# Performance work log

Measured on AMD Instinct MI355X. Metric: run time of the kernel, lower is better.

## Reference

```python
import jax, jax.numpy as jnp
import numpy as np

CLIP_LEN = 16
IN_CH = 64  # math.ceil(256 // 4 / 4) * 4
BN_EPS = 1e-5


def setup_inputs() -> dict:
    key = jax.random.key(0)
    ks = jax.random.split(key, 7)
    x = jax.random.normal(ks[0], (128, 256, 56, 56), jnp.float32)
    bn_gamma = 1.0 + 0.1 * jax.random.normal(ks[1], (IN_CH,), jnp.float32)
    bn_beta = 0.1 * jax.random.normal(ks[2], (IN_CH,), jnp.float32)
    bn_mean = 0.1 * jax.random.normal(ks[3], (IN_CH,), jnp.float32)
    bn_var = jax.random.uniform(ks[4], (IN_CH,), jnp.float32, minval=0.5, maxval=1.5)
    # groups=2 Conv3d: out=2, in_per_group=IN_CH//2, kernel 3x3x3
    conv_w = 0.02 * jax.random.normal(ks[5], (2, IN_CH // 2, 3, 3, 3), jnp.float32)
    conv_b = 0.02 * jax.random.normal(ks[6], (2,), jnp.float32)
    return dict(x=x, bn_gamma=bn_gamma, bn_beta=bn_beta, bn_mean=bn_mean,
                bn_var=bn_var, conv_w=conv_w, conv_b=conv_b)


def _gsm(x5, bn_gamma, bn_beta, bn_mean, bn_var, conv_w, conv_b):
    # x5: [n, c, t, h, w] with c == IN_CH
    n, c, t, h, w = x5.shape
    scale = bn_gamma * jax.lax.rsqrt(bn_var + BN_EPS)          # [c]
    shift = bn_beta - bn_mean * scale                          # [c]
    x_act = jax.nn.relu(x5 * scale[None, :, None, None, None]
                        + shift[None, :, None, None, None])
    gate = jnp.tanh(
        jax.lax.conv_general_dilated(
            x_act, conv_w, window_strides=(1, 1, 1), padding='SAME',
            dimension_numbers=('NCDHW', 'OIDHW', 'NCDHW'),
            feature_group_count=2)
        + conv_b[None, :, None, None, None])                   # [n,2,t,h,w]
    half = c // 2

    def gated_shift(xg, g, left):
        y = g * xg                                             # gated part
        r = xg - y                                             # residual part
        if left:
            y_sh = jnp.concatenate([y[:, :, 1:], jnp.zeros_like(y[:, :, :1])], axis=2)
        else:
            y_sh = jnp.concatenate([jnp.zeros_like(y[:, :, :1]), y[:, :, :-1]], axis=2)
        out = y_sh + r
        # channel regroup: [n,2,c/4,t,h,w] -> permute -> [n,c/2,t,h,w]
        return out.reshape(n, 2, half // 2, t, h, w).transpose(0, 2, 1, 3, 4, 5).reshape(n, half, t, h, w)

    y1 = gated_shift(x5[:, :half], gate[:, 0:1], left=True)
    y2 = gated_shift(x5[:, half:], gate[:, 1:2], left=False)
    return jnp.concatenate([y1, y2], axis=1)


def reference(x, bn_gamma, bn_beta, bn_mean, bn_var, conv_w, conv_b):
    nt, c, h, w = x.shape
    n = nt // CLIP_LEN
    # [nt, IN_CH, h, w] -> [n, IN_CH, T, h, w]
    xs = x[:, :IN_CH].reshape(n, CLIP_LEN, IN_CH, h, w).transpose(0, 2, 1, 3, 4)
    y = _gsm(xs, bn_gamma, bn_beta, bn_mean, bn_var, conv_w, conv_b)
    y = y.transpose(0, 2, 1, 3, 4).reshape(nt, IN_CH, h, w)
    # remaining channels pass through unchanged; net wrapper is identity
    return jnp.concatenate([y, x[:, IN_CH:]], axis=1)
```

## Files before the change

### kernel.cpp

```cpp
#include <hip/hip_runtime.h>
#include <math.h>

namespace {
constexpr int kT = 16;
constexpr int kH = 56;
constexpr int kW = 56;
constexpr int kCAll = 256;
constexpr int kPlane = kH * kW;
constexpr int kPlane4 = kPlane / 4;
constexpr size_t kGateBytes = (size_t)256 * kPlane * sizeof(float);
constexpr int kSpan = 192 * kPlane4;
constexpr int kFrame4 = kCAll * kPlane4;
}


__global__ __launch_bounds__(256, 2)
void fused_conv_copy_kernel(const float* __restrict__ x,
                            const float* __restrict__ gamma,
                            const float* __restrict__ beta,
                            const float* __restrict__ mean,
                            const float* __restrict__ var,
                            const float* __restrict__ cw,
                            const float* __restrict__ cb,
                            float* __restrict__ gate,
                            const float4* __restrict__ x4,
                            float4* __restrict__ o4,
                            int nf_copy, int skip_hole) {
  __shared__ float4 smb[4 * 510];

  if ((blockIdx.x & 1) == 0) {
    const int engine = blockIdx.x >> 1;
    const size_t stride = (size_t)512 * 256;
    const size_t total = (size_t)nf_copy * kSpan;
    size_t j = (size_t)engine * 256 + threadIdx.x;
    auto mapidx = [&](size_t jj, size_t& idx, bool& ok) {
      const int f = (int)(jj / kSpan);
      const int within = (int)(jj - (size_t)f * kSpan);
      ok = !(skip_hole && f == 126 && within < 3 * kPlane4);
      idx = (size_t)f * kFrame4 + 64 * kPlane4 + within;
    };
    for (; j + 3 * stride < total; j += 4 * stride) {
      size_t i0, i1, i2, i3; bool k0, k1, k2, k3;
      mapidx(j, i0, k0); mapidx(j + stride, i1, k1);
      mapidx(j + 2 * stride, i2, k2); mapidx(j + 3 * stride, i3, k3);
      const float4 a = x4[i0], b = x4[i1], c = x4[i2], d = x4[i3];
      if (k0) o4[i0] = a;
      if (k1) o4[i1] = b;
      if (k2) o4[i2] = c;
      if (k3) o4[i3] = d;
    }
    for (; j < total; j += stride) {
      size_t i0; bool k0;
      mapidx(j, i0, k0);
      const float4 a = x4[i0];
      if (k0) o4[i0] = a;
    }
    return;
  }

  const int bid = blockIdx.x >> 1;
  const int stripe = bid & 1;
  const int g = (bid >> 1) & 1;
  const int t = (bid >> 2) & 15;
  const int n = bid >> 6;
  const int h0 = stripe * 28;
  const int tid = threadIdx.x;
  const int wid = tid >> 6;
  const int lane = tid & 63;
  const int r = lane >> 1;
  const int h = lane & 1;
  const int wbase = wid * 510;

  for (int i = lane; i < 510; i += 64)
    smb[wbase + i] = make_float4(0.f, 0.f, 0.f, 0.f);

  int rr_u[7], fb_u[7], go_u[7];
  bool val_u[7];
  #pragma unroll
  for (int u = 0; u < 7; ++u) {
    const int j = lane + u * 64;
    bool v = (j < 420);
    int rr = 0, fb = 0, go = 0;
    if (v) {
      rr = j / 14;
      fb = j - rr * 14;
      const int gr = h0 + rr - 1;
      v = ((unsigned)gr < (unsigned)kH);
      if (v) go = gr * 14 + fb;
    }
    rr_u[u] = rr; fb_u[u] = fb; go_u[u] = go; val_u[u] = v;
  }

  float acc[28];
  #pragma unroll
  for (int p = 0; p < 28; ++p) acc[p] = 0.f;

  auto loadS = [&](int s, float4 (&pf)[7]) {
    const int il = s / 3;
    const int kd = s - il * 3;
    const int tt = t + kd - 1;
    const int ch = g * 32 + wid * 8 + il;
    if (tt >= 0 && tt < kT) {
      const float4* src4 =
          (const float4*)x + ((size_t)(n * kT + tt) * kCAll + ch) * kPlane4;
      #pragma unroll
      for (int u = 0; u < 7; ++u)
        pf[u] = val_u[u] ? src4[go_u[u]] : make_float4(0.f, 0.f, 0.f, 0.f);
    } else {
      #pragma unroll
      for (int u = 0; u < 7; ++u) pf[u] = make_float4(0.f, 0.f, 0.f, 0.f);
    }
  };

  auto stageS = [&](int s, const float4 (&pf)[7]) {
    const int il = s / 3;
    const int kd = s - il * 3;
    const int tt = t + kd - 1;
    if (tt < 0 || tt >= kT) return;
    const int ch = g * 32 + wid * 8 + il;
    const float sc = gamma[ch] * rsqrtf(var[ch] + 1e-5f);
    const float sh = beta[ch] - mean[ch] * sc;
    #pragma unroll
    for (int u = 0; u < 7; ++u) {
      if (val_u[u]) {
        float4 a = pf[u];
        a.x = fmaxf(0.f, fmaf(a.x, sc, sh));
        a.y = fmaxf(0.f, fmaf(a.y, sc, sh));
        a.z = fmaxf(0.f, fmaf(a.z, sc, sh));
        a.w = fmaxf(0.f, fmaf(a.w, sc, sh));
        smb[wbase + rr_u[u] * 17 + fb_u[u] + 1] = a;
      }
    }
  };

  auto computeS = [&](int s) {
    const int il = s / 3;
    const int kd = s - il * 3;
    const int tt = t + kd - 1;
    if (tt < 0 || tt >= kT) return;
    if (r >= 28) return;
    const int ch = g * 32 + wid * 8 + il;
    const float* wbp = cw + ch * 27 + kd * 9;
    float wk[9];
    #pragma unroll
    for (int j = 0; j < 9; ++j) wk[j] = wbp[j];
    #pragma unroll
    for (int kh = 0; kh < 3; ++kh) {
      const int base = wbase + (r + kh) * 17 + 7 * h;
      float f[36];
      #pragma unroll
      for (int jj = 0; jj < 9; ++jj) {
        const float4 B = smb[base + jj];
        f[4 * jj + 0] = B.x; f[4 * jj + 1] = B.y;
        f[4 * jj + 2] = B.z; f[4 * jj + 3] = B.w;
      }
      const float w0 = wk[kh * 3 + 0];
      const float w1 = wk[kh * 3 + 1];
      const float w2 = wk[kh * 3 + 2];
      #pragma unroll
      for (int p = 0; p < 28; ++p)
        acc[p] = fmaf(f[p + 3], w0,
                 fmaf(f[p + 4], w1, fmaf(f[p + 5], w2, acc[p])));
    }
  };

  float4 A[7], B[7];
  loadS(0, A);
  for (int s2 = 0; s2 < 24; s2 += 2) {
    if (s2 + 1 < 24) loadS(s2 + 1, B);
    stageS(s2, A);
    computeS(s2);
    if (s2 + 2 < 24) loadS(s2 + 2, A);
    if (s2 + 1 < 24) { stageS(s2 + 1, B); computeS(s2 + 1); }
  }

  __syncthreads();
  float* smf = (float*)smb;
  if (r < 28) {
    const int q0 = r * 56 + h * 28;
    #pragma unroll
    for (int p = 0; p < 28; ++p) smf[wid * 1568 + q0 + p] = acc[p];
  }
  __syncthreads();
  const float bias = cb[g];
  float* gp = gate + ((size_t)(n * 2 + g) * kT + t) * kPlane + h0 * kW;
  for (int q = tid; q < 1568; q += 256) {
    float s = smf[q] + smf[1568 + q] + smf[2 * 1568 + q] + smf[3 * 1568 + q];
    gp[q] = tanhf(s + bias);
  }
}

__global__ __launch_bounds__(256)
void copy_gate_slice_kernel(float4* __restrict__ o4) {
  const int j = blockIdx.x * 256 + threadIdx.x;
  if (j >= 3 * kPlane4) return;
  const int q = j / kPlane4;
  const int rr = j - q * kPlane4;
  const int pidx = (q == 0) ? 239 : (q == 1 ? 254 : 255);
  const size_t G1 = (size_t)127 * kCAll * kPlane4;
  const size_t H = ((size_t)126 * kCAll + 64) * kPlane4;
  o4[H + j] = o4[G1 + (size_t)pidx * kPlane4 + rr];
}

__global__ __launch_bounds__(256)
void shift_c64_kernel(const float4* __restrict__ x4,
                      const float4* __restrict__ g4,
                      float4* __restrict__ o4, int nf) {
  const size_t total = (size_t)nf * 64 * kPlane4;
  const size_t j = (size_t)blockIdx.x * 256 + threadIdx.x;
  if (j >= total) return;

  const int p = (int)(j % kPlane4);
  const size_t rest = j / kPlane4;
  const int c = (int)(rest % 64);
  const int f = (int)(rest / 64);

  const int n = f >> 4;
  const int t = f & 15;
  const int half = c >> 5;
  const int k = c & 31;
  const int m = ((k & 1) << 4) + (k >> 1);
  const int src_ch = half * 32 + m;

  const size_t xcur = ((size_t)f * kCAll + src_ch) * kPlane4 + p;
  const size_t gbase = (size_t)(n * 2 + half) * kT * kPlane4 + p;

  const float4 xc = x4[xcur];
  const float4 gc = g4[gbase + (size_t)t * kPlane4];
  float4 y = make_float4(0.f, 0.f, 0.f, 0.f);
  if (half == 0) {
    if (t < kT - 1) {
      const float4 xn = x4[xcur + (size_t)kCAll * kPlane4];
      const float4 gn = g4[gbase + (size_t)(t + 1) * kPlane4];
      y.x = gn.x * xn.x; y.y = gn.y * xn.y; y.z = gn.z * xn.z; y.w = gn.w * xn.w;
    }
  } else {
    if (t > 0) {
      const float4 xp = x4[xcur - (size_t)kCAll * kPlane4];
      const float4 gp = g4[gbase + (size_t)(t - 1) * kPlane4];
      y.x = gp.x * xp.x; y.y = gp.y * xp.y; y.z = gp.z * xp.z; y.w = gp.w * xp.w;
    }
  }
  const size_t oidx = ((size_t)f * kCAll + c) * kPlane4 + p;
  float4 res;
  res.x = y.x + (xc.x - gc.x * xc.x);
  res.y = y.y + (xc.y - gc.y * xc.y);
  res.z = y.z + (xc.z - gc.z * xc.z);
  res.w = y.w + (xc.w - gc.w * xc.w);
  o4[oidx] = res;
}

__global__ __launch_bounds__(256)
void last_frame_kernel(const float4* __restrict__ x4,
                       float4* o4) {
  const int idx = blockIdx.x * 256 + threadIdx.x;
  if (idx >= kCAll * kPlane4) return;
  const size_t F127 = (size_t)127 * kCAll * kPlane4;
  const int p = idx % kPlane4;
  const int c = idx / kPlane4;
  if (c >= 64) { o4[F127 + idx] = x4[F127 + idx]; return; }

  const size_t H = ((size_t)126 * kCAll + 64) * kPlane4;
  const int half = c >> 5;
  const int k = c & 31;
  const int m = ((k & 1) << 4) + (k >> 1);
  const int src_ch = half * 32 + m;

  const float4 xc = x4[F127 + (size_t)src_ch * kPlane4 + p];
  float4 gc;
  float4 y = make_float4(0.f, 0.f, 0.f, 0.f);
  if (half == 0) {
    gc = o4[H + 0 * kPlane4 + p];
  } else {
    gc = o4[H + 2 * kPlane4 + p];
    const float4 gp = o4[H + 1 * kPlane4 + p];
    const float4 xp = x4[((size_t)126 * kCAll + src_ch) * kPlane4 + p];
    y.x = gp.x * xp.x; y.y = gp.y * xp.y; y.z = gp.z * xp.z; y.w = gp.w * xp.w;
  }
  float4 res;
  res.x = y.x + (xc.x - gc.x * xc.x);
  res.y = y.y + (xc.y - gc.y * xc.y);
  res.z = y.z + (xc.z - gc.z * xc.z);
  res.w = y.w + (xc.w - gc.w * xc.w);
  o4[F127 + idx] = res;
}

__global__ __launch_bounds__(256)
void fix_hole_kernel(const float4* __restrict__ x4, float4* __restrict__ o4) {
  const int j = blockIdx.x * 256 + threadIdx.x;
  if (j >= 3 * kPlane4) return;
  const size_t H = ((size_t)126 * kCAll + 64) * kPlane4;
  o4[H + j] = x4[H + j];
}

extern "C" void kernel_launch(void* const* d_in, const int* in_sizes, int n_in,
                              void* d_out, int out_size, void* d_ws, size_t ws_size,
                              hipStream_t stream) {
  const float* x     = (const float*)d_in[0];
  const float* gamma = (const float*)d_in[1];
  const float* beta  = (const float*)d_in[2];
  const float* mean  = (const float*)d_in[3];
  const float* var   = (const float*)d_in[4];
  const float* cw    = (const float*)d_in[5];
  const float* cb    = (const float*)d_in[6];
  float* out = (float*)d_out;

  const bool use_ws = (d_ws != nullptr) && (ws_size >= kGateBytes);
  float* gate = use_ws ? (float*)d_ws : out + (size_t)127 * kCAll * kPlane;
  const int nf = use_ws ? 128 : 127;
  const int skip_hole = use_ws ? 0 : 1;

  fused_conv_copy_kernel<<<1024, 256, 0, stream>>>(
      x, gamma, beta, mean, var, cw, cb, gate,
      (const float4*)x, (float4*)out, nf, skip_hole);

  if (!use_ws)
    copy_gate_slice_kernel<<<10, 256, 0, stream>>>((float4*)out);

  const int shift_total = nf * 64 * kPlane4;
  shift_c64_kernel<<<(shift_total + 255) / 256, 256, 0, stream>>>(
      (const float4*)x, (const float4*)gate, (float4*)out, nf);

  if (!use_ws) {
    last_frame_kernel<<<(kCAll * kPlane4 + 255) / 256, 256, 0, stream>>>(
        (const float4*)x, (float4*)out);
    fix_hole_kernel<<<10, 256, 0, stream>>>((const float4*)x, (float4*)out);
  }
}
```

Measured before the change: 216.5 us.

## Fuse conv, copy and shift into one cooperative kernel with grid sync

Adds a cooperative kernel that runs the conv-gate and pass-through copy blocks, performs a grid-wide sync, then does the gated temporal shift in the same launch. The shift is restructured so each thread walks all 16 time steps of one column, reusing the loaded x and gate values across neighbouring frames instead of reloading them. This removes a kernel launch boundary and redundant neighbour loads. In exchange it needs all 1024 blocks co-resident, raises launch_bounds to 4 blocks per CU, and adds grid-sync cost; it falls back to the old path when occupancy or the workspace is insufficient.

```diff
diff --git a/kernel.cpp b/kernel.cpp
--- a/kernel.cpp
+++ b/kernel.cpp
@@ -1,5 +1,8 @@
 #include <hip/hip_runtime.h>
+#include <hip/hip_cooperative_groups.h>
 #include <math.h>
+
+namespace cg = cooperative_groups;
 
 namespace {
 constexpr int kT = 16;
@@ -14,57 +17,17 @@
 }
 
 
-__global__ __launch_bounds__(256, 2)
-void fused_conv_copy_kernel(const float* __restrict__ x,
-                            const float* __restrict__ gamma,
-                            const float* __restrict__ beta,
-                            const float* __restrict__ mean,
-                            const float* __restrict__ var,
-                            const float* __restrict__ cw,
-                            const float* __restrict__ cb,
-                            float* __restrict__ gate,
-                            const float4* __restrict__ x4,
-                            float4* __restrict__ o4,
-                            int nf_copy, int skip_hole) {
-  __shared__ float4 smb[4 * 510];
-
-  if ((blockIdx.x & 1) == 0) {
-    const int engine = blockIdx.x >> 1;
-    const size_t stride = (size_t)512 * 256;
-    const size_t total = (size_t)nf_copy * kSpan;
-    size_t j = (size_t)engine * 256 + threadIdx.x;
-    auto mapidx = [&](size_t jj, size_t& idx, bool& ok) {
-      const int f = (int)(jj / kSpan);
-      const int within = (int)(jj - (size_t)f * kSpan);
-      ok = !(skip_hole && f == 126 && within < 3 * kPlane4);
-      idx = (size_t)f * kFrame4 + 64 * kPlane4 + within;
-    };
-    for (; j + 3 * stride < total; j += 4 * stride) {
-      size_t i0, i1, i2, i3; bool k0, k1, k2, k3;
-      mapidx(j, i0, k0); mapidx(j + stride, i1, k1);
-      mapidx(j + 2 * stride, i2, k2); mapidx(j + 3 * stride, i3, k3);
-      const float4 a = x4[i0], b = x4[i1], c = x4[i2], d = x4[i3];
-      if (k0) o4[i0] = a;
-      if (k1) o4[i1] = b;
-      if (k2) o4[i2] = c;
-      if (k3) o4[i3] = d;
-    }
-    for (; j < total; j += stride) {
-      size_t i0; bool k0;
-      mapidx(j, i0, k0);
-      const float4 a = x4[i0];
-      if (k0) o4[i0] = a;
-    }
-    return;
-  }
-
-  const int bid = blockIdx.x >> 1;
+__device__ __forceinline__ void conv_block(
+    int bid, int tid, const float* __restrict__ x,
+    const float* __restrict__ gamma, const float* __restrict__ beta,
+    const float* __restrict__ mean, const float* __restrict__ var,
+    const float* __restrict__ cw, const float* __restrict__ cb,
+    float* __restrict__ gate, float4* smb) {
   const int stripe = bid & 1;
   const int g = (bid >> 1) & 1;
   const int t = (bid >> 2) & 15;
   const int n = bid >> 6;
   const int h0 = stripe * 28;
-  const int tid = threadIdx.x;
   const int wid = tid >> 6;
   const int lane = tid & 63;
   const int r = lane >> 1;
@@ -190,6 +153,129 @@
   }
 }
 
+__device__ __forceinline__ void copy_engine(
+    int engine, int nengines, int tid, const float4* __restrict__ x4,
+    float4* __restrict__ o4, int nf, int skip_hole) {
+  const size_t stride = (size_t)nengines * 256;
+  const size_t total = (size_t)nf * kSpan;
+  size_t j = (size_t)engine * 256 + tid;
+  auto mapidx = [&](size_t jj, size_t& idx, bool& ok) {
+    const int f = (int)(jj / kSpan);
+    const int within = (int)(jj - (size_t)f * kSpan);
+    ok = !(skip_hole && f == 126 && within < 3 * kPlane4);
+    idx = (size_t)f * kFrame4 + 64 * kPlane4 + within;
+  };
+  for (; j + 3 * stride < total; j += 4 * stride) {
+    size_t i0, i1, i2, i3; bool k0, k1, k2, k3;
+    mapidx(j, i0, k0); mapidx(j + stride, i1, k1);
+    mapidx(j + 2 * stride, i2, k2); mapidx(j + 3 * stride, i3, k3);
+    const float4 a = x4[i0], b = x4[i1], c = x4[i2], d = x4[i3];
+    if (k0) o4[i0] = a;
+    if (k1) o4[i1] = b;
+    if (k2) o4[i2] = c;
+    if (k3) o4[i3] = d;
+  }
+  for (; j < total; j += stride) {
+    size_t i0; bool k0;
+    mapidx(j, i0, k0);
+    const float4 a = x4[i0];
+    if (k0) o4[i0] = a;
+  }
+}
+
+__device__ __forceinline__ void shift_columns(
+    int q0, int qstride, const float4* __restrict__ x4,
+    const float4* __restrict__ g4, float4* __restrict__ o4) {
+  const size_t xstep = (size_t)kFrame4;
+  for (int q = q0; q < 8 * 2 * 32 * kPlane4; q += qstride) {
+    const int p = q % kPlane4;
+    const int rem = q / kPlane4;
+    const int m = rem & 31;
+    const int half = (rem >> 5) & 1;
+    const int n = rem >> 6;
+    const int src_ch = half * 32 + m;
+    const int k = 2 * (m & 15) + (m >> 4);
+    const int c = half * 32 + k;
+    const float4* xp = x4 + ((size_t)(n * kT) * kCAll + src_ch) * kPlane4 + p;
+    const float4* gp = g4 + (size_t)((n * 2 + half) * kT) * kPlane4 + p;
+    float4* op = o4 + ((size_t)(n * kT) * kCAll + c) * kPlane4 + p;
+    if (half == 0) {
+      float4 xc = xp[0], gc = gp[0];
+      #pragma unroll
+      for (int t = 0; t < kT; ++t) {
+        float4 xn = make_float4(0.f, 0.f, 0.f, 0.f);
+        float4 gn = make_float4(0.f, 0.f, 0.f, 0.f);
+        if (t < kT - 1) { xn = xp[(size_t)(t + 1) * xstep]; gn = gp[(t + 1) * kPlane4]; }
+        float4 res;
+        res.x = gn.x * xn.x + xc.x - gc.x * xc.x;
+        res.y = gn.y * xn.y + xc.y - gc.y * xc.y;
+        res.z = gn.z * xn.z + xc.z - gc.z * xc.z;
+        res.w = gn.w * xn.w + xc.w - gc.w * xc.w;
+        op[(size_t)t * xstep] = res;
+        xc = xn; gc = gn;
+      }
+    } else {
+      float4 xprev = make_float4(0.f, 0.f, 0.f, 0.f);
+      float4 gprev = make_float4(0.f, 0.f, 0.f, 0.f);
+      #pragma unroll
+      for (int t = 0; t < kT; ++t) {
+        const float4 xc = xp[(size_t)t * xstep];
+        const float4 gc = gp[t * kPlane4];
+        float4 res;
+        res.x = gprev.x * xprev.x + xc.x - gc.x * xc.x;
+        res.y = gprev.y * xprev.y + xc.y - gc.y * xc.y;
+        res.z = gprev.z * xprev.z + xc.z - gc.z * xc.z;
+        res.w = gprev.w * xprev.w + xc.w - gc.w * xc.w;
+        op[(size_t)t * xstep] = res;
+        xprev = xc; gprev = gc;
+      }
+    }
+  }
+}
+
+__global__ __launch_bounds__(256, 4)
+void coop_fused_kernel(const float* __restrict__ x,
+                       const float* __restrict__ gamma,
+                       const float* __restrict__ beta,
+                       const float* __restrict__ mean,
+                       const float* __restrict__ var,
+                       const float* __restrict__ cw,
+                       const float* __restrict__ cb,
+                       float* __restrict__ gate,
+                       const float4* __restrict__ x4,
+                       float4* __restrict__ o4) {
+  __shared__ float4 smb[4 * 510];
+  if (blockIdx.x & 1)
+    conv_block(blockIdx.x >> 1, threadIdx.x, x, gamma, beta, mean, var, cw, cb,
+               gate, smb);
+  else
+    copy_engine(blockIdx.x >> 1, 512, threadIdx.x, x4, o4, 128, 0);
+  cg::this_grid().sync();
+  shift_columns(blockIdx.x * 256 + threadIdx.x, 1024 * 256, x4,
+                (const float4*)gate, o4);
+}
+
+__global__ __launch_bounds__(256, 2)
+void fused_conv_copy_kernel(const float* __restrict__ x,
+                            const float* __restrict__ gamma,
+                            const float* __restrict__ beta,
+                            const float* __restrict__ mean,
+                            const float* __restrict__ var,
+                            const float* __restrict__ cw,
+                            const float* __restrict__ cb,
+                            float* __restrict__ gate,
+                            const float4* __restrict__ x4,
+                            float4* __restrict__ o4,
+                            int nf_copy, int skip_hole) {
+  __shared__ float4 smb[4 * 510];
+  if ((blockIdx.x & 1) == 0) {
+    copy_engine(blockIdx.x >> 1, 512, threadIdx.x, x4, o4, nf_copy, skip_hole);
+    return;
+  }
+  conv_block(blockIdx.x >> 1, threadIdx.x, x, gamma, beta, mean, var, cw, cb,
+             gate, smb);
+}
+
 __global__ __launch_bounds__(256)
 void copy_gate_slice_kernel(float4* __restrict__ o4) {
   const int j = blockIdx.x * 256 + threadIdx.x;
@@ -209,22 +295,18 @@
   const size_t total = (size_t)nf * 64 * kPlane4;
   const size_t j = (size_t)blockIdx.x * 256 + threadIdx.x;
   if (j >= total) return;
-
   const int p = (int)(j % kPlane4);
   const size_t rest = j / kPlane4;
   const int c = (int)(rest % 64);
   const int f = (int)(rest / 64);
-
   const int n = f >> 4;
   const int t = f & 15;
   const int half = c >> 5;
   const int k = c & 31;
   const int m = ((k & 1) << 4) + (k >> 1);
   const int src_ch = half * 32 + m;
-
   const size_t xcur = ((size_t)f * kCAll + src_ch) * kPlane4 + p;
   const size_t gbase = (size_t)(n * 2 + half) * kT * kPlane4 + p;
-
   const float4 xc = x4[xcur];
   const float4 gc = g4[gbase + (size_t)t * kPlane4];
   float4 y = make_float4(0.f, 0.f, 0.f, 0.f);
@@ -251,21 +333,18 @@
 }
 
 __global__ __launch_bounds__(256)
-void last_frame_kernel(const float4* __restrict__ x4,
-                       float4* o4) {
+void last_frame_kernel(const float4* __restrict__ x4, float4* o4) {
   const int idx = blockIdx.x * 256 + threadIdx.x;
   if (idx >= kCAll * kPlane4) return;
   const size_t F127 = (size_t)127 * kCAll * kPlane4;
   const int p = idx % kPlane4;
   const int c = idx / kPlane4;
   if (c >= 64) { o4[F127 + idx] = x4[F127 + idx]; return; }
-
   const size_t H = ((size_t)126 * kCAll + 64) * kPlane4;
   const int half = c >> 5;
   const int k = c & 31;
   const int m = ((k & 1) << 4) + (k >> 1);
   const int src_ch = half * 32 + m;
-
   const float4 xc = x4[F127 + (size_t)src_ch * kPlane4 + p];
   float4 gc;
   float4 y = make_float4(0.f, 0.f, 0.f, 0.f);
@@ -304,26 +383,42 @@
   const float* cw    = (const float*)d_in[5];
   const float* cb    = (const float*)d_in[6];
   float* out = (float*)d_out;
-
-  const bool use_ws = (d_ws != nullptr) && (ws_size >= kGateBytes);
-  float* gate = use_ws ? (float*)d_ws : out + (size_t)127 * kCAll * kPlane;
-  const int nf = use_ws ? 128 : 127;
-  const int skip_hole = use_ws ? 0 : 1;
+  const float4* x4v = (const float4*)x;
+  float4* o4v = (float4*)out;
+
+  const bool have_ws = (d_ws != nullptr) && (ws_size >= kGateBytes);
+
+  if (have_ws) {
+    int maxBlocks = 0;
+    hipError_t qe = hipOccupancyMaxActiveBlocksPerMultiprocessor(
+        &maxBlocks, (const void*)coop_fused_kernel, 256, 0);
+    if (qe == hipSuccess && maxBlocks >= 4) {
+      float* gate = (float*)d_ws;
+      void* args[] = {(void*)&x, (void*)&gamma, (void*)&beta, (void*)&mean,
+                      (void*)&var, (void*)&cw, (void*)&cb, (void*)&gate,
+                      (void*)&x4v, (void*)&o4v};
+      hipError_t le = hipLaunchCooperativeKernel(
+          (const void*)coop_fused_kernel, dim3(1024), dim3(256), args, 0, stream);
+      if (le == hipSuccess) return;
+    }
+  }
+
+  float* gate = have_ws ? (float*)d_ws : out + (size_t)127 * kCAll * kPlane;
+  const int nf = have_ws ? 128 : 127;
+  const int skip_hole = have_ws ? 0 : 1;
 
   fused_conv_copy_kernel<<<1024, 256, 0, stream>>>(
-      x, gamma, beta, mean, var, cw, cb, gate,
-      (const float4*)x, (float4*)out, nf, skip_hole);
-
-  if (!use_ws)
-    copy_gate_slice_kernel<<<10, 256, 0, stream>>>((float4*)out);
+      x, gamma, beta, mean, var, cw, cb, gate, x4v, o4v, nf, skip_hole);
+
+  if (!have_ws)
+    copy_gate_slice_kernel<<<10, 256, 0, stream>>>(o4v);
 
   const int shift_total = nf * 64 * kPlane4;
   shift_c64_kernel<<<(shift_total + 255) / 256, 256, 0, stream>>>(
-      (const float4*)x, (const float4*)gate, (float4*)out, nf);
-
-  if (!use_ws) {
-    last_frame_kernel<<<(kCAll * kPlane4 + 255) / 256, 256, 0, stream>>>(
-        (const float4*)x, (float4*)out);
-    fix_hole_kernel<<<10, 256, 0, stream>>>((const float4*)x, (float4*)out);
-  }
-}
+      x4v, (const float4*)gate, o4v, nf);
+
+  if (!have_ws) {
+    last_frame_kernel<<<(kCAll * kPlane4 + 255) / 256, 256, 0, stream>>>(x4v, o4v);
+    fix_hole_kernel<<<10, 256, 0, stream>>>(x4v, o4v);
+  }
+}
```

Result: no change. 216.5 us (-0.0%).
